# Kernel optimization log

Hardware: AMD Instinct MI355X
Metric: run time of the kernel (lower is better)

Reference implementation:

```python
import jax, jax.numpy as jnp
import numpy as np
from jax import lax

B, T, E, D, A, C, FILT = 32, 1600, 1024, 1024, 512, 10, 100
SCALING = 2.0


def setup_inputs() -> dict:
    key = jax.random.key(0)
    ks = jax.random.split(key, 14)
    enc_hs_pad = jax.random.normal(ks[0], (B, T, E), dtype=jnp.float32)
    # lengths in [T//2, T] so every row has valid positions
    enc_hs_len = jax.random.randint(ks[1], (B,), T // 2, T + 1, dtype=jnp.int32)
    dec_z = jax.random.normal(ks[2], (B, D), dtype=jnp.float32)
    # previous attention weights: uniform over valid frames, normalized
    valid = (jnp.arange(T)[None, :] < enc_hs_len[:, None]).astype(jnp.float32)
    raw = jax.random.uniform(ks[3], (B, T), dtype=jnp.float32) * valid
    att_prev = raw / jnp.sum(raw, axis=1, keepdims=True)
    att_h = 0.1 * jax.random.normal(ks[4], (B, A), dtype=jnp.float32)
    att_c = 0.1 * jax.random.normal(ks[5], (B, A), dtype=jnp.float32)
    W_enc = jax.random.normal(ks[6], (A, E), dtype=jnp.float32) / np.sqrt(E)
    b_enc = jax.random.normal(ks[7], (A,), dtype=jnp.float32) * 0.01
    W_dec = jax.random.normal(ks[8], (A, D), dtype=jnp.float32) / np.sqrt(D)
    conv_w = jax.random.normal(ks[9], (C, 1, 2 * FILT + 1), dtype=jnp.float32) / np.sqrt(2 * FILT + 1)
    W_ih = jax.random.normal(ks[10], (4 * A, C), dtype=jnp.float32) / np.sqrt(C)
    W_hh = jax.random.normal(ks[11], (4 * A, A), dtype=jnp.float32) / np.sqrt(A)
    W_g = jax.random.normal(ks[12], (A,), dtype=jnp.float32) / np.sqrt(A)
    b_g = jnp.zeros((1,), dtype=jnp.float32)
    return {"enc_hs_pad": enc_hs_pad, "enc_hs_len": enc_hs_len, "dec_z": dec_z,
            "att_prev": att_prev, "att_h": att_h, "att_c": att_c,
            "W_enc": W_enc, "b_enc": b_enc, "W_dec": W_dec, "conv_w": conv_w,
            "W_ih": W_ih, "W_hh": W_hh, "W_g": W_g, "b_g": b_g}


def reference(enc_hs_pad, enc_hs_len, dec_z, att_prev, att_h, att_c,
              W_enc, b_enc, W_dec, conv_w, W_ih, W_hh, W_g, b_g):
    t_len = enc_hs_pad.shape[1]
    filts = (conv_w.shape[-1] - 1) // 2

    # precompute encoder projection (B, T, A)
    pre_enc = jnp.einsum('bte,ae->bta', enc_hs_pad, W_enc) + b_enc

    # location conv on previous attention: (B,1,T) -> (B,C,T), relu, global max-pool over T
    att_conv = lax.conv_general_dilated(att_prev[:, None, :], conv_w,
                                        window_strides=(1,), padding=[(filts, filts)],
                                        dimension_numbers=('NCH', 'OIH', 'NCH'))
    att_feat = jnp.max(jax.nn.relu(att_conv), axis=-1)  # (B, C)

    # LSTMCell (no bias), pytorch gate order i, f, g, o
    gates = att_feat @ W_ih.T + att_h @ W_hh.T  # (B, 4A)
    i, f, g, o = jnp.split(gates, 4, axis=-1)
    c_new = jax.nn.sigmoid(f) * att_c + jax.nn.sigmoid(i) * jnp.tanh(g)
    h_new = jax.nn.sigmoid(o) * jnp.tanh(c_new)  # (B, A)

    dec_proj = dec_z @ W_dec.T  # (B, A)
    # scores (B, T)
    e = jnp.tanh(h_new[:, None, :] + pre_enc + dec_proj[:, None, :]) @ W_g + b_g

    mask = jnp.arange(t_len)[None, :] >= enc_hs_len[:, None]  # True = pad
    e = jnp.where(mask, jnp.finfo(e.dtype).min, e)
    w = jax.nn.softmax(SCALING * e, axis=1)  # (B, T)

    ctx = jnp.einsum('bt,bte->be', w, enc_hs_pad)  # (B, E)
    return ctx, w, h_new, c_new
```

## Files before the change

kernel.cpp:

```cpp
#include <hip/hip_runtime.h>
#include <hip/hip_bf16.h>

#define BB 32
#define TT 1600
#define EE 1024
#define AA 512
#define CC 10
#define KW 201

typedef __attribute__((ext_vector_type(8))) short short8;
typedef __attribute__((ext_vector_type(4))) float f32x4;

__device__ __forceinline__ float sigm(float x) { return 1.f / (1.f + expf(-x)); }

__device__ __forceinline__ unsigned int cvt2(float a, float b) {
    float2 f2; f2.x = a; f2.y = b;
    __hip_bfloat162 h = __float22bfloat162_rn(f2);
    unsigned int r;
    __builtin_memcpy(&r, &h, 4);
    return r;
}

__device__ __forceinline__ void gl_lds16(const void* g, void* l) {
    __builtin_amdgcn_global_load_lds(
        (const __attribute__((address_space(1))) unsigned int*)g,
        (__attribute__((address_space(3))) unsigned int*)l, 16, 0, 0);
}

#define AF_OFF    0
#define GATES_OFF 320
#define DEC_OFF   65856
#define R_OFF     82240
#define E_OFF     98624
#define WBF_OFF   149824

#define CTX_OFF 0
#define W_OFF   32768
#define H_OFF   83968
#define C_OFF   100352

__global__ void zero_kernel(float* out, float* af, float* e_ws) {
    int i = blockIdx.x * 256 + threadIdx.x;
    if (i < 32768) out[CTX_OFF + i] = 0.f;
    else if (i < 33088) af[i - 32768] = 0.f;
    else if (i < 84288) e_ws[i - 33088] = 0.f;
}

__global__ void wconv_kernel(const float* __restrict__ W_enc, unsigned short* __restrict__ Wbf) {
    int i = blockIdx.x * 256 + threadIdx.x;
    float4 v = reinterpret_cast<const float4*>(W_enc)[i];
    uint2 p;
    p.x = cvt2(v.x, v.y);
    p.y = cvt2(v.z, v.w);
    reinterpret_cast<uint2*>(Wbf)[i] = p;
}

__global__ void conv_kernel(const float* __restrict__ att_prev,
                            const float* __restrict__ conv_w,
                            unsigned int* __restrict__ af) {
    int b = blockIdx.x, c = blockIdx.y, seg = blockIdx.z;
    int ts = seg * 400;
    __shared__ float x[600];
    __shared__ float wsm[KW];
    __shared__ float red[256];
    int tid = threadIdx.x;
    const float* xp = att_prev + b * TT;
    for (int i = tid; i < 600; i += 256) {
        int g = ts - 100 + i;
        x[i] = (g >= 0 && g < TT) ? xp[g] : 0.f;
    }
    if (tid < KW) wsm[tid] = conv_w[c * KW + tid];
    __syncthreads();
    float mx = 0.f;
    for (int tt = tid; tt < 400; tt += 256) {
        float s = 0.f;
        #pragma unroll 4
        for (int k = 0; k < KW; ++k) s += wsm[k] * x[tt + k];
        mx = fmaxf(mx, s);
    }
    red[tid] = mx; __syncthreads();
    for (int s = 128; s > 0; s >>= 1) {
        if (tid < s) red[tid] = fmaxf(red[tid], red[tid + s]);
        __syncthreads();
    }
    if (tid == 0) atomicMax(&af[b * CC + c], __float_as_uint(red[0]));
}

__global__ void small_gemm_kernel(const float* __restrict__ af,
                                  const float* __restrict__ att_h,
                                  const float* __restrict__ dec_z,
                                  const float* __restrict__ W_ih,
                                  const float* __restrict__ W_hh,
                                  const float* __restrict__ W_dec,
                                  float* __restrict__ gates,
                                  float* __restrict__ dec_proj) {
    int tid = threadIdx.x;
    int b = tid & 31, jl = tid >> 5;
    int j = blockIdx.x * 8 + jl;
    if (j < 2048) {
        float s = 0.f;
        #pragma unroll
        for (int k = 0; k < 10; ++k) s += af[b * 10 + k] * W_ih[j * 10 + k];
        const float4* hh4 = reinterpret_cast<const float4*>(W_hh + (size_t)j * 512);
        const float4* h4  = reinterpret_cast<const float4*>(att_h + b * 512);
        #pragma unroll 4
        for (int k = 0; k < 128; ++k) {
            float4 a = h4[k], w = hh4[k];
            s += a.x * w.x + a.y * w.y + a.z * w.z + a.w * w.w;
        }
        gates[b * 2048 + j] = s;
    } else {
        int a = j - 2048;
        const float4* wd4 = reinterpret_cast<const float4*>(W_dec + (size_t)a * 1024);
        const float4* z4  = reinterpret_cast<const float4*>(dec_z + b * 1024);
        float s = 0.f;
        #pragma unroll 4
        for (int k = 0; k < 256; ++k) {
            float4 a4 = z4[k], w = wd4[k];
            s += a4.x * w.x + a4.y * w.y + a4.z * w.z + a4.w * w.w;
        }
        dec_proj[b * 512 + a] = s;
    }
}

__global__ void lstm_kernel(const float* __restrict__ gates,
                            const float* __restrict__ att_c,
                            const float* __restrict__ dec_proj,
                            float* __restrict__ out,
                            float* __restrict__ r) {
    int idx = blockIdx.x * 256 + threadIdx.x;
    int b = idx >> 9, a = idx & 511;
    const float* g = gates + b * 2048;
    float ig = g[a], fg = g[512 + a], gg = g[1024 + a], og = g[1536 + a];
    float cn = sigm(fg) * att_c[idx] + sigm(ig) * tanhf(gg);
    float hn = sigm(og) * tanhf(cn);
    out[H_OFF + idx] = hn;
    out[C_OFF + idx] = cn;
    r[idx] = hn + dec_proj[idx];
}

__global__ void __launch_bounds__(256, 2)
score_gemm_kernel(const float* __restrict__ enc,
                  const unsigned short* __restrict__ Wbf,
                  const float* __restrict__ b_enc,
                  const float* __restrict__ r_ws,
                  const float* __restrict__ W_g,
                  float* __restrict__ e_ws) {
    __shared__ __align__(16) short As[128 * 32];
    __shared__ __align__(16) short Bs[128 * 32];

    int tid = threadIdx.x;
    int lane = tid & 63, wv = tid >> 6;
    int col = lane & 15, quad = lane >> 4;
    int wm = wv >> 1, wn = wv & 1;
    int n0 = blockIdx.x * 128;
    int m0 = blockIdx.y * 128;

    int arow = tid >> 1, ahalf = (tid & 1) * 16;
    const float* abase = enc + (size_t)(m0 + arow) * EE + ahalf;

    f32x4 acc[4][4];
    #pragma unroll
    for (int mt = 0; mt < 4; ++mt)
        #pragma unroll
        for (int nt = 0; nt < 4; ++nt)
            acc[mt][nt] = (f32x4){0.f, 0.f, 0.f, 0.f};

    for (int k0 = 0; k0 < EE; k0 += 32) {
        const float4* ag = reinterpret_cast<const float4*>(abase + k0);
        float4 v0 = ag[0], v1 = ag[1], v2 = ag[2], v3 = ag[3];

        __syncthreads();

        {
            int c = tid;
            gl_lds16(Wbf + (size_t)(n0 + (c >> 2)) * EE + k0 + (c & 3) * 8, Bs + c * 8);
            c = tid + 256;
            gl_lds16(Wbf + (size_t)(n0 + (c >> 2)) * EE + k0 + (c & 3) * 8, Bs + c * 8);
        }
        int4 st0, st1;
        st0.x = cvt2(v0.x, v0.y); st0.y = cvt2(v0.z, v0.w);
        st0.z = cvt2(v1.x, v1.y); st0.w = cvt2(v1.z, v1.w);
        st1.x = cvt2(v2.x, v2.y); st1.y = cvt2(v2.z, v2.w);
        st1.z = cvt2(v3.x, v3.y); st1.w = cvt2(v3.z, v3.w);
        *reinterpret_cast<int4*>(&As[arow * 32 + ahalf]) = st0;
        *reinterpret_cast<int4*>(&As[arow * 32 + ahalf + 8]) = st1;

        __syncthreads();

        short8 a_frag[4];
        #pragma unroll
        for (int mt = 0; mt < 4; ++mt)
            a_frag[mt] = *reinterpret_cast<const short8*>(
                &As[(wm * 64 + mt * 16 + col) * 32 + quad * 8]);
        #pragma unroll
        for (int nt = 0; nt < 4; ++nt) {
            short8 b_frag = *reinterpret_cast<const short8*>(
                &Bs[(wn * 64 + nt * 16 + col) * 32 + quad * 8]);
            #pragma unroll
            for (int mt = 0; mt < 4; ++mt)
                acc[mt][nt] = __builtin_amdgcn_mfma_f32_16x16x32_bf16(
                    a_frag[mt], b_frag, acc[mt][nt], 0, 0, 0);
        }
    }

    int n_base = n0 + wn * 64;
    float wg[4], bn[4];
    #pragma unroll
    for (int nt = 0; nt < 4; ++nt) {
        int n = n_base + nt * 16 + col;
        wg[nt] = W_g[n];
        bn[nt] = b_enc[n];
    }
    #pragma unroll
    for (int mt = 0; mt < 4; ++mt) {
        int mg = m0 + wm * 64 + mt * 16;
        int bb = mg / TT;
        float rn[4];
        #pragma unroll
        for (int nt = 0; nt < 4; ++nt)
            rn[nt] = r_ws[bb * AA + n_base + nt * 16 + col];
        #pragma unroll
        for (int reg = 0; reg < 4; ++reg) {
            float p = 0.f;
            #pragma unroll
            for (int nt = 0; nt < 4; ++nt)
                p += wg[nt] * tanhf(acc[mt][nt][reg] + bn[nt] + rn[nt]);
            p += __shfl_xor(p, 1);
            p += __shfl_xor(p, 2);
            p += __shfl_xor(p, 4);
            p += __shfl_xor(p, 8);
            if (col == 0) atomicAdd(&e_ws[mg + quad * 4 + reg], p);
        }
    }
}

__global__ void softmax_kernel(const float* __restrict__ e_ws,
                               const int* __restrict__ lens,
                               float* __restrict__ w_out) {
    int b = blockIdx.x, tid = threadIdx.x;
    int len = lens[b];
    const float* e = e_ws + b * TT;
    __shared__ float red[256];
    float mx = -3.4e38f;
    for (int t = tid; t < len; t += 256) mx = fmaxf(mx, e[t]);
    red[tid] = mx; __syncthreads();
    for (int s = 128; s > 0; s >>= 1) {
        if (tid < s) red[tid] = fmaxf(red[tid], red[tid + s]);
        __syncthreads();
    }
    mx = red[0]; __syncthreads();
    float sum = 0.f;
    for (int t = tid; t < len; t += 256) sum += expf(2.f * (e[t] - mx));
    red[tid] = sum; __syncthreads();
    for (int s = 128; s > 0; s >>= 1) {
        if (tid < s) red[tid] += red[tid + s];
        __syncthreads();
    }
    float inv = 1.f / red[0];
    for (int t = tid; t < TT; t += 256)
        w_out[b * TT + t] = (t < len) ? expf(2.f * (e[t] - mx)) * inv : 0.f;
}

__global__ void ctx_kernel(const float* __restrict__ enc,
                           const float* __restrict__ w,
                           float* __restrict__ ctx) {
    int b = blockIdx.x, seg = blockIdx.y;
    int t0 = seg * 100;
    const float* wrow = w + b * TT + t0;
    const float* base = enc + ((size_t)(b * TT + t0)) * EE + threadIdx.x * 4;
    float4 acc = {0.f, 0.f, 0.f, 0.f};
    #pragma unroll 1
    for (int i = 0; i < 100; i += 4) {
        float w0 = wrow[i], w1 = wrow[i + 1], w2 = wrow[i + 2], w3 = wrow[i + 3];
        float4 v0 = *reinterpret_cast<const float4*>(base + (size_t)(i + 0) * EE);
        float4 v1 = *reinterpret_cast<const float4*>(base + (size_t)(i + 1) * EE);
        float4 v2 = *reinterpret_cast<const float4*>(base + (size_t)(i + 2) * EE);
        float4 v3 = *reinterpret_cast<const float4*>(base + (size_t)(i + 3) * EE);
        acc.x += w0 * v0.x + w1 * v1.x + w2 * v2.x + w3 * v3.x;
        acc.y += w0 * v0.y + w1 * v1.y + w2 * v2.y + w3 * v3.y;
        acc.z += w0 * v0.z + w1 * v1.z + w2 * v2.z + w3 * v3.z;
        acc.w += w0 * v0.w + w1 * v1.w + w2 * v2.w + w3 * v3.w;
    }
    float* dst = ctx + b * EE + threadIdx.x * 4;
    atomicAdd(dst + 0, acc.x);
    atomicAdd(dst + 1, acc.y);
    atomicAdd(dst + 2, acc.z);
    atomicAdd(dst + 3, acc.w);
}

extern "C" void kernel_launch(void* const* d_in, const int* in_sizes, int n_in,
                              void* d_out, int out_size, void* d_ws, size_t ws_size,
                              hipStream_t stream) {
    const float* enc      = (const float*)d_in[0];
    const int*   lens     = (const int*)d_in[1];
    const float* dec_z    = (const float*)d_in[2];
    const float* att_prev = (const float*)d_in[3];
    const float* att_h    = (const float*)d_in[4];
    const float* att_c    = (const float*)d_in[5];
    const float* W_enc    = (const float*)d_in[6];
    const float* b_enc    = (const float*)d_in[7];
    const float* W_dec    = (const float*)d_in[8];
    const float* conv_w   = (const float*)d_in[9];
    const float* W_ih     = (const float*)d_in[10];
    const float* W_hh     = (const float*)d_in[11];
    const float* W_g      = (const float*)d_in[12];

    float* out = (float*)d_out;
    float* ws  = (float*)d_ws;
    float* af        = ws + AF_OFF;
    float* gates     = ws + GATES_OFF;
    float* dec_proj  = ws + DEC_OFF;
    float* r_ws      = ws + R_OFF;
    float* e_ws      = ws + E_OFF;
    unsigned short* Wbf = (unsigned short*)(ws + WBF_OFF);

    zero_kernel<<<330, 256, 0, stream>>>(out, af, e_ws);
    wconv_kernel<<<512, 256, 0, stream>>>(W_enc, Wbf);
    conv_kernel<<<dim3(BB, CC, 4), 256, 0, stream>>>(att_prev, conv_w, (unsigned int*)af);
    small_gemm_kernel<<<320, 256, 0, stream>>>(af, att_h, dec_z, W_ih, W_hh, W_dec,
                                               gates, dec_proj);
    lstm_kernel<<<64, 256, 0, stream>>>(gates, att_c, dec_proj, out, r_ws);
    score_gemm_kernel<<<dim3(4, 400), 256, 0, stream>>>(enc, Wbf, b_enc, r_ws, W_g, e_ws);
    softmax_kernel<<<BB, 256, 0, stream>>>(e_ws, lens, out + W_OFF);
    ctx_kernel<<<dim3(BB, 16), 256, 0, stream>>>(enc, out + W_OFF, out + CTX_OFF);
}
```

Measured before the change: 524.8 us.

## Fuse pipeline into four kernels and retile score GEMM for full-N blocks

Merges zeroing, weight conversion and conv into one prep kernel. Fuses the small GEMMs with the LSTM cell, and softmax with the context reduction, which removes the atomics and the zero-init pass. The score GEMM now uses 1024-thread blocks that each cover all 512 attention columns. This lets each encoder tile be read and converted to bf16 once rather than four times, with double-buffered LDS and an in-block reduction of the scores. The cost is larger blocks and LDS use, which lowers occupancy, and less parallelism in the fused small kernels.

```diff
diff --git a/kernel.cpp b/kernel.cpp
--- a/kernel.cpp
+++ b/kernel.cpp
@@ -27,266 +27,307 @@
         (__attribute__((address_space(3))) unsigned int*)l, 16, 0, 0);
 }
 
-#define AF_OFF    0
-#define GATES_OFF 320
-#define DEC_OFF   65856
-#define R_OFF     82240
-#define E_OFF     98624
-#define WBF_OFF   149824
+#define AF_OFF   0
+#define R_OFF    320
+#define E_OFF    16704
+#define WBF_OFF  67904
 
 #define CTX_OFF 0
 #define W_OFF   32768
 #define H_OFF   83968
 #define C_OFF   100352
 
-__global__ void zero_kernel(float* out, float* af, float* e_ws) {
-    int i = blockIdx.x * 256 + threadIdx.x;
-    if (i < 32768) out[CTX_OFF + i] = 0.f;
-    else if (i < 33088) af[i - 32768] = 0.f;
-    else if (i < 84288) e_ws[i - 33088] = 0.f;
-}
-
-__global__ void wconv_kernel(const float* __restrict__ W_enc, unsigned short* __restrict__ Wbf) {
-    int i = blockIdx.x * 256 + threadIdx.x;
-    float4 v = reinterpret_cast<const float4*>(W_enc)[i];
-    uint2 p;
-    p.x = cvt2(v.x, v.y);
-    p.y = cvt2(v.z, v.w);
-    reinterpret_cast<uint2*>(Wbf)[i] = p;
-}
-
-__global__ void conv_kernel(const float* __restrict__ att_prev,
+__global__ void prep_kernel(const float* __restrict__ att_prev,
                             const float* __restrict__ conv_w,
-                            unsigned int* __restrict__ af) {
-    int b = blockIdx.x, c = blockIdx.y, seg = blockIdx.z;
-    int ts = seg * 400;
-    __shared__ float x[600];
+                            const float* __restrict__ W_enc,
+                            float* __restrict__ af,
+                            unsigned short* __restrict__ Wbf) {
+    int bx = blockIdx.x, tid = threadIdx.x;
+    if (bx >= 320) {
+        int i = (bx - 320) * 256 + tid;
+        float4 v = reinterpret_cast<const float4*>(W_enc)[i];
+        uint2 p;
+        p.x = cvt2(v.x, v.y);
+        p.y = cvt2(v.z, v.w);
+        reinterpret_cast<uint2*>(Wbf)[i] = p;
+        return;
+    }
+    int b = bx / 10, c = bx % 10;
+    __shared__ float xs[1808];
     __shared__ float wsm[KW];
     __shared__ float red[256];
-    int tid = threadIdx.x;
     const float* xp = att_prev + b * TT;
-    for (int i = tid; i < 600; i += 256) {
-        int g = ts - 100 + i;
-        x[i] = (g >= 0 && g < TT) ? xp[g] : 0.f;
+    for (int i = tid; i < 1808; i += 256) {
+        int g = i - 100;
+        xs[i] = (g >= 0 && g < TT) ? xp[g] : 0.f;
     }
     if (tid < KW) wsm[tid] = conv_w[c * KW + tid];
     __syncthreads();
     float mx = 0.f;
-    for (int tt = tid; tt < 400; tt += 256) {
-        float s = 0.f;
+    #pragma unroll 1
+    for (int sweep = 0; sweep < 2; ++sweep) {
+        int t0 = sweep * 1024 + tid * 4;
+        if (t0 >= TT) break;
+        float a0 = xs[t0], a1 = xs[t0 + 1], a2 = xs[t0 + 2], a3 = xs[t0 + 3];
+        float s0 = 0.f, s1 = 0.f, s2 = 0.f, s3 = 0.f;
         #pragma unroll 4
-        for (int k = 0; k < KW; ++k) s += wsm[k] * x[tt + k];
-        mx = fmaxf(mx, s);
+        for (int k = 0; k < KW; ++k) {
+            float w = wsm[k];
+            s0 += w * a0; s1 += w * a1; s2 += w * a2; s3 += w * a3;
+            a0 = a1; a1 = a2; a2 = a3;
+            a3 = xs[t0 + k + 4];
+        }
+        mx = fmaxf(mx, fmaxf(fmaxf(s0, s1), fmaxf(s2, s3)));
     }
     red[tid] = mx; __syncthreads();
     for (int s = 128; s > 0; s >>= 1) {
         if (tid < s) red[tid] = fmaxf(red[tid], red[tid + s]);
         __syncthreads();
     }
-    if (tid == 0) atomicMax(&af[b * CC + c], __float_as_uint(red[0]));
-}
-
-__global__ void small_gemm_kernel(const float* __restrict__ af,
+    if (tid == 0) af[b * CC + c] = red[0];
+}
+
+__global__ void gates_lstm_kernel(const float* __restrict__ af,
                                   const float* __restrict__ att_h,
                                   const float* __restrict__ dec_z,
+                                  const float* __restrict__ att_c,
                                   const float* __restrict__ W_ih,
                                   const float* __restrict__ W_hh,
                                   const float* __restrict__ W_dec,
-                                  float* __restrict__ gates,
-                                  float* __restrict__ dec_proj) {
+                                  float* __restrict__ out,
+                                  float* __restrict__ r_ws) {
+    __shared__ float gsm[8][32];
+    __shared__ float dsm[8][32];
     int tid = threadIdx.x;
-    int b = tid & 31, jl = tid >> 5;
-    int j = blockIdx.x * 8 + jl;
-    if (j < 2048) {
+    int a0 = blockIdx.x * 2;
+    int b = tid & 31;
+    if (tid < 256) {
+        int u = tid >> 5;
+        int gate = u >> 1, ai = u & 1;
+        int j = gate * 512 + a0 + ai;
         float s = 0.f;
         #pragma unroll
         for (int k = 0; k < 10; ++k) s += af[b * 10 + k] * W_ih[j * 10 + k];
-        const float4* hh4 = reinterpret_cast<const float4*>(W_hh + (size_t)j * 512);
-        const float4* h4  = reinterpret_cast<const float4*>(att_h + b * 512);
+        const float4* wr = reinterpret_cast<const float4*>(W_hh + (size_t)j * 512);
+        const float4* hr = reinterpret_cast<const float4*>(att_h + b * 512);
         #pragma unroll 4
         for (int k = 0; k < 128; ++k) {
-            float4 a = h4[k], w = hh4[k];
-            s += a.x * w.x + a.y * w.y + a.z * w.z + a.w * w.w;
-        }
-        gates[b * 2048 + j] = s;
+            float4 w = wr[k], h = hr[k];
+            s += w.x * h.x + w.y * h.y + w.z * h.z + w.w * h.w;
+        }
+        gsm[u][b] = s;
     } else {
-        int a = j - 2048;
-        const float4* wd4 = reinterpret_cast<const float4*>(W_dec + (size_t)a * 1024);
-        const float4* z4  = reinterpret_cast<const float4*>(dec_z + b * 1024);
+        int v = (tid - 256) >> 5;
+        int ai = v & 1, q = v >> 1;
+        int a = a0 + ai;
+        const float4* wr = reinterpret_cast<const float4*>(W_dec + (size_t)a * 1024) + q * 64;
+        const float4* zr = reinterpret_cast<const float4*>(dec_z + (size_t)b * 1024) + q * 64;
         float s = 0.f;
         #pragma unroll 4
-        for (int k = 0; k < 256; ++k) {
-            float4 a4 = z4[k], w = wd4[k];
-            s += a4.x * w.x + a4.y * w.y + a4.z * w.z + a4.w * w.w;
-        }
-        dec_proj[b * 512 + a] = s;
-    }
-}
-
-__global__ void lstm_kernel(const float* __restrict__ gates,
-                            const float* __restrict__ att_c,
-                            const float* __restrict__ dec_proj,
-                            float* __restrict__ out,
-                            float* __restrict__ r) {
-    int idx = blockIdx.x * 256 + threadIdx.x;
-    int b = idx >> 9, a = idx & 511;
-    const float* g = gates + b * 2048;
-    float ig = g[a], fg = g[512 + a], gg = g[1024 + a], og = g[1536 + a];
-    float cn = sigm(fg) * att_c[idx] + sigm(ig) * tanhf(gg);
-    float hn = sigm(og) * tanhf(cn);
-    out[H_OFF + idx] = hn;
-    out[C_OFF + idx] = cn;
-    r[idx] = hn + dec_proj[idx];
-}
-
-__global__ void __launch_bounds__(256, 2)
+        for (int k = 0; k < 64; ++k) {
+            float4 w = wr[k], z = zr[k];
+            s += w.x * z.x + w.y * z.y + w.z * z.z + w.w * z.w;
+        }
+        dsm[v][b] = s;
+    }
+    __syncthreads();
+    if (tid < 64) {
+        int ai = tid >> 5;
+        int a = a0 + ai;
+        float ig = gsm[ai][b], fg = gsm[2 + ai][b], gg = gsm[4 + ai][b], og = gsm[6 + ai][b];
+        float cn = sigm(fg) * att_c[b * 512 + a] + sigm(ig) * tanhf(gg);
+        float hn = sigm(og) * tanhf(cn);
+        out[H_OFF + b * 512 + a] = hn;
+        out[C_OFF + b * 512 + a] = cn;
+        float dec = dsm[ai][b] + dsm[2 + ai][b] + dsm[4 + ai][b] + dsm[6 + ai][b];
+        r_ws[b * 512 + a] = hn + dec;
+    }
+}
+
+__global__ void __launch_bounds__(1024, 4)
 score_gemm_kernel(const float* __restrict__ enc,
                   const unsigned short* __restrict__ Wbf,
                   const float* __restrict__ b_enc,
                   const float* __restrict__ r_ws,
                   const float* __restrict__ W_g,
                   float* __restrict__ e_ws) {
-    __shared__ __align__(16) short As[128 * 32];
-    __shared__ __align__(16) short Bs[128 * 32];
+    __shared__ __align__(16) short As[2][4096];
+    __shared__ __align__(16) short Bs[2][8192];
+    __shared__ float e_part[8][128];
 
     int tid = threadIdx.x;
     int lane = tid & 63, wv = tid >> 6;
+    int wm = wv >> 3, wn = wv & 7;
     int col = lane & 15, quad = lane >> 4;
-    int wm = wv >> 1, wn = wv & 1;
-    int n0 = blockIdx.x * 128;
-    int m0 = blockIdx.y * 128;
-
-    int arow = tid >> 1, ahalf = (tid & 1) * 16;
-    const float* abase = enc + (size_t)(m0 + arow) * EE + ahalf;
-
-    f32x4 acc[4][4];
+    int m0 = blockIdx.x * 128;
+
+    const unsigned short* bsrc = Wbf + (size_t)((tid >> 6) * 16 + (tid & 15)) * EE
+                                 + ((tid >> 4) & 3) * 8;
+    int arow = tid >> 3, akq2 = tid & 7;
+    const float* asrc = enc + (size_t)(m0 + arow) * EE + akq2 * 4;
+    int adst = (arow >> 4) * 512 + ((akq2 >> 1) * 16 + (arow & 15)) * 8 + (akq2 & 1) * 4;
+
+    f32x4 acc[4][2][2];
     #pragma unroll
     for (int mt = 0; mt < 4; ++mt)
         #pragma unroll
-        for (int nt = 0; nt < 4; ++nt)
-            acc[mt][nt] = (f32x4){0.f, 0.f, 0.f, 0.f};
-
+        for (int h = 0; h < 2; ++h)
+            #pragma unroll
+            for (int nt = 0; nt < 2; ++nt)
+                acc[mt][h][nt] = (f32x4){0.f, 0.f, 0.f, 0.f};
+
+    {
+        gl_lds16(bsrc, &Bs[0][tid * 8]);
+        float4 v = *reinterpret_cast<const float4*>(asrc);
+        uint2 p; p.x = cvt2(v.x, v.y); p.y = cvt2(v.z, v.w);
+        *reinterpret_cast<uint2*>(&As[0][adst]) = p;
+    }
+    __syncthreads();
+
+    int bufA = 0;
     for (int k0 = 0; k0 < EE; k0 += 32) {
-        const float4* ag = reinterpret_cast<const float4*>(abase + k0);
-        float4 v0 = ag[0], v1 = ag[1], v2 = ag[2], v3 = ag[3];
-
-        __syncthreads();
-
-        {
-            int c = tid;
-            gl_lds16(Wbf + (size_t)(n0 + (c >> 2)) * EE + k0 + (c & 3) * 8, Bs + c * 8);
-            c = tid + 256;
-            gl_lds16(Wbf + (size_t)(n0 + (c >> 2)) * EE + k0 + (c & 3) * 8, Bs + c * 8);
-        }
-        int4 st0, st1;
-        st0.x = cvt2(v0.x, v0.y); st0.y = cvt2(v0.z, v0.w);
-        st0.z = cvt2(v1.x, v1.y); st0.w = cvt2(v1.z, v1.w);
-        st1.x = cvt2(v2.x, v2.y); st1.y = cvt2(v2.z, v2.w);
-        st1.z = cvt2(v3.x, v3.y); st1.w = cvt2(v3.z, v3.w);
-        *reinterpret_cast<int4*>(&As[arow * 32 + ahalf]) = st0;
-        *reinterpret_cast<int4*>(&As[arow * 32 + ahalf + 8]) = st1;
-
-        __syncthreads();
-
+        bool last = (k0 == EE - 32);
+        gl_lds16(bsrc + (size_t)256 * EE + k0, &Bs[1][tid * 8]);
         short8 a_frag[4];
         #pragma unroll
         for (int mt = 0; mt < 4; ++mt)
             a_frag[mt] = *reinterpret_cast<const short8*>(
-                &As[(wm * 64 + mt * 16 + col) * 32 + quad * 8]);
-        #pragma unroll
-        for (int nt = 0; nt < 4; ++nt) {
-            short8 b_frag = *reinterpret_cast<const short8*>(
-                &Bs[(wn * 64 + nt * 16 + col) * 32 + quad * 8]);
+                &As[bufA][(wm * 4 + mt) * 512 + (quad * 16 + col) * 8]);
+        #pragma unroll
+        for (int nt = 0; nt < 2; ++nt) {
+            short8 bf = *reinterpret_cast<const short8*>(
+                &Bs[0][(wn * 2 + nt) * 512 + (quad * 16 + col) * 8]);
             #pragma unroll
             for (int mt = 0; mt < 4; ++mt)
-                acc[mt][nt] = __builtin_amdgcn_mfma_f32_16x16x32_bf16(
-                    a_frag[mt], b_frag, acc[mt][nt], 0, 0, 0);
-        }
-    }
-
-    int n_base = n0 + wn * 64;
-    float wg[4], bn[4];
+                acc[mt][0][nt] = __builtin_amdgcn_mfma_f32_16x16x32_bf16(
+                    a_frag[mt], bf, acc[mt][0][nt], 0, 0, 0);
+        }
+        __syncthreads();
+        float4 av;
+        if (!last) {
+            av = *reinterpret_cast<const float4*>(asrc + k0 + 32);
+            gl_lds16(bsrc + k0 + 32, &Bs[0][tid * 8]);
+        }
+        #pragma unroll
+        for (int nt = 0; nt < 2; ++nt) {
+            short8 bf = *reinterpret_cast<const short8*>(
+                &Bs[1][(wn * 2 + nt) * 512 + (quad * 16 + col) * 8]);
+            #pragma unroll
+            for (int mt = 0; mt < 4; ++mt)
+                acc[mt][1][nt] = __builtin_amdgcn_mfma_f32_16x16x32_bf16(
+                    a_frag[mt], bf, acc[mt][1][nt], 0, 0, 0);
+        }
+        if (!last) {
+            uint2 p; p.x = cvt2(av.x, av.y); p.y = cvt2(av.z, av.w);
+            *reinterpret_cast<uint2*>(&As[bufA ^ 1][adst]) = p;
+        }
+        __syncthreads();
+        bufA ^= 1;
+    }
+
+    float wg[2][2], bn[2][2];
     #pragma unroll
-    for (int nt = 0; nt < 4; ++nt) {
-        int n = n_base + nt * 16 + col;
-        wg[nt] = W_g[n];
-        bn[nt] = b_enc[n];
-    }
+    for (int h = 0; h < 2; ++h)
+        #pragma unroll
+        for (int nt = 0; nt < 2; ++nt) {
+            int n = h * 256 + wn * 32 + nt * 16 + col;
+            wg[h][nt] = W_g[n];
+            bn[h][nt] = b_enc[n];
+        }
     #pragma unroll
     for (int mt = 0; mt < 4; ++mt) {
         int mg = m0 + wm * 64 + mt * 16;
         int bb = mg / TT;
-        float rn[4];
-        #pragma unroll
-        for (int nt = 0; nt < 4; ++nt)
-            rn[nt] = r_ws[bb * AA + n_base + nt * 16 + col];
+        float rr[2][2];
+        #pragma unroll
+        for (int h = 0; h < 2; ++h)
+            #pragma unroll
+            for (int nt = 0; nt < 2; ++nt)
+                rr[h][nt] = r_ws[bb * AA + h * 256 + wn * 32 + nt * 16 + col];
         #pragma unroll
         for (int reg = 0; reg < 4; ++reg) {
             float p = 0.f;
             #pragma unroll
-            for (int nt = 0; nt < 4; ++nt)
-                p += wg[nt] * tanhf(acc[mt][nt][reg] + bn[nt] + rn[nt]);
+            for (int h = 0; h < 2; ++h)
+                #pragma unroll
+                for (int nt = 0; nt < 2; ++nt)
+                    p += wg[h][nt] * tanhf(acc[mt][h][nt][reg] + bn[h][nt] + rr[h][nt]);
             p += __shfl_xor(p, 1);
             p += __shfl_xor(p, 2);
             p += __shfl_xor(p, 4);
             p += __shfl_xor(p, 8);
-            if (col == 0) atomicAdd(&e_ws[mg + quad * 4 + reg], p);
-        }
-    }
-}
-
-__global__ void softmax_kernel(const float* __restrict__ e_ws,
-                               const int* __restrict__ lens,
-                               float* __restrict__ w_out) {
-    int b = blockIdx.x, tid = threadIdx.x;
+            if (col == 0) e_part[wn][wm * 64 + mt * 16 + quad * 4 + reg] = p;
+        }
+    }
+    __syncthreads();
+    if (tid < 128) {
+        float s = 0.f;
+        #pragma unroll
+        for (int i = 0; i < 8; ++i) s += e_part[i][tid];
+        e_ws[m0 + tid] = s;
+    }
+}
+
+__global__ void ctx_softmax_kernel(const float* __restrict__ enc,
+                                   const float* __restrict__ e_ws,
+                                   const int* __restrict__ lens,
+                                   float* __restrict__ w_out,
+                                   float* __restrict__ ctx) {
+    int b = blockIdx.x, ch = blockIdx.y;
+    int tid = threadIdx.x;
+    __shared__ float w_sm[1600];
+    __shared__ float red[512];
+    __shared__ float part[8][128];
     int len = lens[b];
     const float* e = e_ws + b * TT;
-    __shared__ float red[256];
     float mx = -3.4e38f;
-    for (int t = tid; t < len; t += 256) mx = fmaxf(mx, e[t]);
+    for (int t = tid; t < len; t += 512) mx = fmaxf(mx, e[t]);
     red[tid] = mx; __syncthreads();
-    for (int s = 128; s > 0; s >>= 1) {
+    for (int s = 256; s > 0; s >>= 1) {
         if (tid < s) red[tid] = fmaxf(red[tid], red[tid + s]);
         __syncthreads();
     }
     mx = red[0]; __syncthreads();
     float sum = 0.f;
-    for (int t = tid; t < len; t += 256) sum += expf(2.f * (e[t] - mx));
+    for (int t = tid; t < TT; t += 512) {
+        float p = (t < len) ? expf(2.f * (e[t] - mx)) : 0.f;
+        w_sm[t] = p; sum += p;
+    }
     red[tid] = sum; __syncthreads();
-    for (int s = 128; s > 0; s >>= 1) {
+    for (int s = 256; s > 0; s >>= 1) {
         if (tid < s) red[tid] += red[tid + s];
         __syncthreads();
     }
     float inv = 1.f / red[0];
-    for (int t = tid; t < TT; t += 256)
-        w_out[b * TT + t] = (t < len) ? expf(2.f * (e[t] - mx)) * inv : 0.f;
-}
-
-__global__ void ctx_kernel(const float* __restrict__ enc,
-                           const float* __restrict__ w,
-                           float* __restrict__ ctx) {
-    int b = blockIdx.x, seg = blockIdx.y;
-    int t0 = seg * 100;
-    const float* wrow = w + b * TT + t0;
-    const float* base = enc + ((size_t)(b * TT + t0)) * EE + threadIdx.x * 4;
-    float4 acc = {0.f, 0.f, 0.f, 0.f};
+    __syncthreads();
+    for (int t = tid; t < TT; t += 512) {
+        float wv = w_sm[t] * inv;
+        w_sm[t] = wv;
+        if (ch == 0) w_out[b * TT + t] = wv;
+    }
+    __syncthreads();
+    int lane2 = tid & 63, w8 = tid >> 6;
+    int tb = w8 * 200;
+    const float* base = enc + (size_t)(b * TT + tb) * EE + ch * 128 + lane2 * 2;
+    float cx = 0.f, cy = 0.f;
     #pragma unroll 1
-    for (int i = 0; i < 100; i += 4) {
-        float w0 = wrow[i], w1 = wrow[i + 1], w2 = wrow[i + 2], w3 = wrow[i + 3];
-        float4 v0 = *reinterpret_cast<const float4*>(base + (size_t)(i + 0) * EE);
-        float4 v1 = *reinterpret_cast<const float4*>(base + (size_t)(i + 1) * EE);
-        float4 v2 = *reinterpret_cast<const float4*>(base + (size_t)(i + 2) * EE);
-        float4 v3 = *reinterpret_cast<const float4*>(base + (size_t)(i + 3) * EE);
-        acc.x += w0 * v0.x + w1 * v1.x + w2 * v2.x + w3 * v3.x;
-        acc.y += w0 * v0.y + w1 * v1.y + w2 * v2.y + w3 * v3.y;
-        acc.z += w0 * v0.z + w1 * v1.z + w2 * v2.z + w3 * v3.z;
-        acc.w += w0 * v0.w + w1 * v1.w + w2 * v2.w + w3 * v3.w;
-    }
-    float* dst = ctx + b * EE + threadIdx.x * 4;
-    atomicAdd(dst + 0, acc.x);
-    atomicAdd(dst + 1, acc.y);
-    atomicAdd(dst + 2, acc.z);
-    atomicAdd(dst + 3, acc.w);
+    for (int i = 0; i < 200; i += 8) {
+        #pragma unroll
+        for (int j = 0; j < 8; ++j) {
+            float2 v = *reinterpret_cast<const float2*>(base + (size_t)(i + j) * EE);
+            float ww = w_sm[tb + i + j];
+            cx += ww * v.x; cy += ww * v.y;
+        }
+    }
+    part[w8][lane2 * 2] = cx;
+    part[w8][lane2 * 2 + 1] = cy;
+    __syncthreads();
+    if (tid < 128) {
+        float s = 0.f;
+        #pragma unroll
+        for (int i = 0; i < 8; ++i) s += part[i][tid];
+        ctx[b * EE + ch * 128 + tid] = s;
+    }
 }
 
 extern "C" void kernel_launch(void* const* d_in, const int* in_sizes, int n_in,
@@ -308,20 +349,15 @@
 
     float* out = (float*)d_out;
     float* ws  = (float*)d_ws;
-    float* af        = ws + AF_OFF;
-    float* gates     = ws + GATES_OFF;
-    float* dec_proj  = ws + DEC_OFF;
-    float* r_ws      = ws + R_OFF;
-    float* e_ws      = ws + E_OFF;
+    float* af   = ws + AF_OFF;
+    float* r_ws = ws + R_OFF;
+    float* e_ws = ws + E_OFF;
     unsigned short* Wbf = (unsigned short*)(ws + WBF_OFF);
 
-    zero_kernel<<<330, 256, 0, stream>>>(out, af, e_ws);
-    wconv_kernel<<<512, 256, 0, stream>>>(W_enc, Wbf);
-    conv_kernel<<<dim3(BB, CC, 4), 256, 0, stream>>>(att_prev, conv_w, (unsigned int*)af);
-    small_gemm_kernel<<<320, 256, 0, stream>>>(af, att_h, dec_z, W_ih, W_hh, W_dec,
-                                               gates, dec_proj);
-    lstm_kernel<<<64, 256, 0, stream>>>(gates, att_c, dec_proj, out, r_ws);
-    score_gemm_kernel<<<dim3(4, 400), 256, 0, stream>>>(enc, Wbf, b_enc, r_ws, W_g, e_ws);
-    softmax_kernel<<<BB, 256, 0, stream>>>(e_ws, lens, out + W_OFF);
-    ctx_kernel<<<dim3(BB, 16), 256, 0, stream>>>(enc, out + W_OFF, out + CTX_OFF);
-}
+    prep_kernel<<<832, 256, 0, stream>>>(att_prev, conv_w, W_enc, af, Wbf);
+    gates_lstm_kernel<<<256, 512, 0, stream>>>(af, att_h, dec_z, att_c,
+                                               W_ih, W_hh, W_dec, out, r_ws);
+    score_gemm_kernel<<<400, 1024, 0, stream>>>(enc, Wbf, b_enc, r_ws, W_g, e_ws);
+    ctx_softmax_kernel<<<dim3(BB, 8), 512, 0, stream>>>(enc, e_ws, lens,
+                                                        out + W_OFF, out + CTX_OFF);
+}
```

New measurement: 497.1 us. 1.06x faster.
